# Optimization experiments

Measured on AMD Instinct MI355X. Metric: run time of the kernel, lower is better.

Reference implementation:

```python
import jax, jax.numpy as jnp
import numpy as np

D_MODEL = 512
NUM_HEADS = 8
DEPTH = D_MODEL // NUM_HEADS
BATCH = 2
SEQ = 2048
NEG_INF_SCALE = -1e9


def setup_inputs() -> dict:
    key = jax.random.key(0)
    ks = jax.random.split(key, 9)
    s = 0.02
    return {
        "v": jax.random.normal(ks[0], (BATCH, SEQ, D_MODEL), jnp.float32),
        "q": jax.random.normal(ks[1], (BATCH, SEQ, D_MODEL), jnp.float32),
        "k": jax.random.normal(ks[2], (BATCH, SEQ, D_MODEL), jnp.float32),
        "mask": jax.random.randint(ks[3], (BATCH, 1, SEQ, SEQ), 0, 2, jnp.int32),
        "wq_w": jax.random.normal(ks[4], (D_MODEL, D_MODEL), jnp.float32) * s,
        "wq_b": jnp.zeros((D_MODEL,), jnp.float32),
        "wk_w": jax.random.normal(ks[5], (D_MODEL, D_MODEL), jnp.float32) * s,
        "wk_b": jnp.zeros((D_MODEL,), jnp.float32),
        "wv_w": jax.random.normal(ks[6], (D_MODEL, D_MODEL), jnp.float32) * s,
        "wv_b": jnp.zeros((D_MODEL,), jnp.float32),
        "wo_w": jax.random.normal(ks[7], (D_MODEL, D_MODEL), jnp.float32) * s,
        "wo_b": jnp.zeros((D_MODEL,), jnp.float32),
    }


def _split_heads(x, b):
    # [b, s, d_model] -> [b, h, s, depth]
    return x.reshape(b, -1, NUM_HEADS, DEPTH).transpose(0, 2, 1, 3)


def reference(v, q, k, mask, wq_w, wq_b, wk_w, wk_b, wv_w, wv_b, wo_w, wo_b):
    b = q.shape[0]
    vv = _split_heads(v @ wv_w + wv_b, b)  # [b,h,s,d]
    kk = _split_heads(k @ wk_w + wk_b, b)
    qq = _split_heads(q @ wq_w + wq_b, b)
    # NOTE: the original code swaps q/k at the helper call site, so logits = K @ Q^T.
    logits = jnp.einsum("bhkd,bhqd->bhkq", kk, qq) / jnp.sqrt(jnp.float32(DEPTH))
    logits = logits + mask.astype(jnp.float32) * NEG_INF_SCALE
    attn = jax.nn.softmax(logits, axis=-1)  # softmax over the query axis (faithful quirk)
    # output = A^T @ V  -> [b,h,q,d]
    out = jnp.einsum("bhkq,bhkd->bhqd", attn, vv)
    concat = out.transpose(0, 2, 1, 3).reshape(b, -1, D_MODEL)
    return concat @ wo_w + wo_b, attn
```

## Files before the change

### kernel.cpp

```cpp
#include <hip/hip_runtime.h>

#define S 2048
#define DM 512
#define NH 8
#define HD 64
#define NB 2
#define BH (NB * NH)
#define MROWS (NB * S)
#define QW (S / 32)

typedef __bf16 bf16x8 __attribute__((ext_vector_type(8)));
typedef float f32x4 __attribute__((ext_vector_type(4)));

union FragU {
  uint4 u;
  bf16x8 v;
  unsigned short s[8];
};

__device__ __forceinline__ unsigned short f2bf(float x) {
  unsigned u = __float_as_uint(x);
  u += 0x7FFFu + ((u >> 16) & 1u);
  return (unsigned short)(u >> 16);
}

__global__ __launch_bounds__(256) void k_prep(
    const float* __restrict__ w0, const float* __restrict__ w1,
    const float* __restrict__ w2, const float* __restrict__ w3,
    unsigned short* __restrict__ wt,
    const float* __restrict__ q, const float* __restrict__ k, const float* __restrict__ v,
    unsigned short* __restrict__ oq, unsigned short* __restrict__ ok, unsigned short* __restrict__ ov,
    const int* __restrict__ mask, unsigned* __restrict__ mp,
    float* __restrict__ Zs) {
  __shared__ float tile[64][65];
  int bid = blockIdx.x;
  int tid = threadIdx.x;
  if (bid < 256) {
    int i = bid >> 6, rem = bid & 63;
    const float* w = (i == 0) ? w0 : (i == 1) ? w1 : (i == 2) ? w2 : w3;
    int k0 = (rem & 7) * 64, n0 = (rem >> 3) * 64;
    int tx = tid & 63, ty = tid >> 6;
    for (int r = ty; r < 64; r += 4)
      tile[r][tx] = w[(size_t)(k0 + r) * DM + n0 + tx];
    __syncthreads();
    unsigned short* o = wt + (size_t)i * DM * DM;
    for (int r = ty; r < 64; r += 4)
      o[(size_t)(n0 + r) * DM + k0 + tx] = f2bf(tile[tx][r]);
  } else if (bid < 3328) {
    int b2 = bid - 256;
    int which = b2 >> 10;
    const float* src = (which == 0) ? q : (which == 1) ? k : v;
    unsigned short* dst = (which == 0) ? oq : (which == 1) ? ok : ov;
    size_t t = (size_t)(b2 & 1023) * 256 + tid;
    const float4* s4 = (const float4*)src + t * 2;
    float4 x = s4[0], y = s4[1];
    FragU f;
    f.s[0] = f2bf(x.x); f.s[1] = f2bf(x.y); f.s[2] = f2bf(x.z); f.s[3] = f2bf(x.w);
    f.s[4] = f2bf(y.x); f.s[5] = f2bf(y.y); f.s[6] = f2bf(y.z); f.s[7] = f2bf(y.w);
    *(uint4*)(dst + t * 8) = f.u;
  } else if (bid < 4352) {
    size_t t = (size_t)(bid - 3328) * 256 + tid;
    const int4* mb = (const int4*)(mask + t * 32);
    unsigned bits = 0;
#pragma unroll
    for (int c = 0; c < 8; c++) {
      int4 m = mb[c];
      bits |= (m.x != 0 ? 1u : 0u) << (c * 4);
      bits |= (m.y != 0 ? 1u : 0u) << (c * 4 + 1);
      bits |= (m.z != 0 ? 1u : 0u) << (c * 4 + 2);
      bits |= (m.w != 0 ? 1u : 0u) << (c * 4 + 3);
    }
    mp[t] = bits;
  } else {
    int t = (bid - 4352) * 256 + tid;
    ((float4*)Zs)[t] = make_float4(0.f, 0.f, 0.f, 0.f);
  }
}

__global__ __launch_bounds__(256) void k_proj(
    const unsigned short* __restrict__ inq, const unsigned short* __restrict__ ink,
    const unsigned short* __restrict__ inv, const unsigned short* __restrict__ wt,
    const float* __restrict__ bq, const float* __restrict__ bk, const float* __restrict__ bv,
    unsigned short* __restrict__ oq, unsigned short* __restrict__ ok,
    unsigned short* __restrict__ vvT) {
  __shared__ __align__(16) unsigned short vt[64][72];
  int which = blockIdx.z;
  const unsigned short* in = (which == 0) ? inq : (which == 1) ? ink : inv;
  const float* bias = (which == 0) ? bq : (which == 1) ? bk : bv;
  const unsigned short* w = wt + (size_t)which * DM * DM;

  int lane = threadIdx.x & 63, wv = threadIdx.x >> 6;
  int m0 = blockIdx.x * 64 + wv * 16;
  int n0 = blockIdx.y * 64;
  int kf = (lane >> 4) * 8;
  int arow = m0 + (lane & 15);

  f32x4 acc[4] = {{0.f, 0.f, 0.f, 0.f}, {0.f, 0.f, 0.f, 0.f},
                  {0.f, 0.f, 0.f, 0.f}, {0.f, 0.f, 0.f, 0.f}};

  for (int kk0 = 0; kk0 < DM; kk0 += 32) {
    FragU af;
    af.u = *(const uint4*)(in + (size_t)arow * DM + kk0 + kf);
#pragma unroll
    for (int nt = 0; nt < 4; nt++) {
      FragU bfr;
      bfr.u = *(const uint4*)(w + (size_t)(n0 + nt * 16 + (lane & 15)) * DM + kk0 + kf);
      acc[nt] = __builtin_amdgcn_mfma_f32_16x16x32_bf16(af.v, bfr.v, acc[nt], 0, 0, 0);
    }
  }

  if (which < 2) {
    unsigned short* out = (which == 0) ? oq : ok;
#pragma unroll
    for (int nt = 0; nt < 4; nt++) {
#pragma unroll
      for (int r = 0; r < 4; r++) {
        int row = m0 + (lane >> 4) * 4 + r;
        int col = n0 + nt * 16 + (lane & 15);
        float val = acc[nt][r] + bias[col];
        int b = row >> 11, sIdx = row & (S - 1);
        int h = col >> 6, d = col & 63;
        out[(((size_t)(b * NH + h) * S) + sIdx) * HD + d] = f2bf(val);
      }
    }
  } else {
#pragma unroll
    for (int nt = 0; nt < 4; nt++) {
#pragma unroll
      for (int r = 0; r < 4; r++) {
        int sl = wv * 16 + (lane >> 4) * 4 + r;
        int dl = nt * 16 + (lane & 15);
        vt[dl][sl] = f2bf(acc[nt][r] + bias[n0 + dl]);
      }
    }
    __syncthreads();
    int b = (blockIdx.x * 64) >> 11;
    int s0l = (blockIdx.x * 64) & (S - 1);
    int h = n0 >> 6;
    unsigned short* op = vvT + (size_t)(b * NH + h) * HD * S;
    int d = threadIdx.x >> 2;
    int sc = (threadIdx.x & 3) * 16;
#pragma unroll
    for (int j = 0; j < 2; j++)
      *(uint4*)&op[(size_t)d * S + s0l + sc + j * 8] = *(uint4*)&vt[d][sc + j * 8];
  }
}

__global__ __launch_bounds__(256, 4) void k_softmax_z(
    const unsigned short* __restrict__ qq, const unsigned short* __restrict__ kk,
    const unsigned* __restrict__ mp, float* __restrict__ Zsum) {
  int lane = threadIdx.x & 63, w = threadIdx.x >> 6;
  int bh = blockIdx.y;
  int b = bh >> 3;
  int k0 = blockIdx.x * 64 + w * 16;
  int kf = (lane >> 4) * 8;
  int qbase = blockIdx.z * (S / 2);
  int krow_b = k0 + (lane >> 4) * 4;

  const unsigned short* kbase = kk + ((size_t)bh * S + k0 + (lane & 15)) * HD + kf;
  FragU a0, a1;
  a0.u = *(const uint4*)kbase;
  a1.u = *(const uint4*)(kbase + 32);

  const unsigned short* qbaseP = qq + (size_t)bh * S * HD;
  const unsigned* mpb = mp + (size_t)b * S * QW;

  float sum[4] = {0.f, 0.f, 0.f, 0.f};

  for (int q0 = qbase; q0 < qbase + S / 2; q0 += 64) {
    uint2 mw[4];
#pragma unroll
    for (int r = 0; r < 4; r++)
      mw[r] = *(const uint2*)&mpb[(size_t)(krow_b + r) * QW + (q0 >> 5)];
#pragma unroll
    for (int nt = 0; nt < 4; nt++) {
      int qcol = q0 + nt * 16 + (lane & 15);
      const unsigned short* qp = qbaseP + (size_t)qcol * HD + kf;
      FragU b0, b1;
      b0.u = *(const uint4*)qp;
      b1.u = *(const uint4*)(qp + 32);
      f32x4 c = {0.f, 0.f, 0.f, 0.f};
      c = __builtin_amdgcn_mfma_f32_16x16x32_bf16(a0.v, b0.v, c, 0, 0, 0);
      c = __builtin_amdgcn_mfma_f32_16x16x32_bf16(a1.v, b1.v, c, 0, 0, 0);
      unsigned bpos = (unsigned)(nt * 16 + (lane & 15)) & 31u;
#pragma unroll
      for (int r = 0; r < 4; r++) {
        unsigned word = (nt < 2) ? mw[r].x : mw[r].y;
        float e = __expf(c[r] * 0.125f);
        sum[r] += ((word >> bpos) & 1u) ? 0.f : e;
      }
    }
  }
#pragma unroll
  for (int r = 0; r < 4; r++) {
    float s = sum[r];
    s += __shfl_xor(s, 1);
    s += __shfl_xor(s, 2);
    s += __shfl_xor(s, 4);
    s += __shfl_xor(s, 8);
    if ((lane & 15) == 0)
      atomicAdd(&Zsum[(size_t)bh * S + krow_b + r], s);
  }
}

__global__ __launch_bounds__(256, 4) void k_attn(
    const unsigned short* __restrict__ qq, const unsigned short* __restrict__ kk,
    const unsigned short* __restrict__ vvT, const unsigned* __restrict__ mp,
    const float* __restrict__ Zsum, float* __restrict__ attn_out,
    float* __restrict__ pO) {
  __shared__ __align__(16) unsigned short pT[2][64][72];
  int lane = threadIdx.x & 63, w = threadIdx.x >> 6;
  int bh = blockIdx.y;
  int b = bh >> 3, h = bh & 7;
  int q0 = blockIdx.x * 64;
  int kbase = blockIdx.z * (S / 2);
  int kf = (lane >> 4) * 8;

  FragU bq[4][2];
#pragma unroll
  for (int nt = 0; nt < 4; nt++) {
    const unsigned short* qp = qq + ((size_t)bh * S + q0 + nt * 16 + (lane & 15)) * HD + kf;
    bq[nt][0].u = *(const uint4*)qp;
    bq[nt][1].u = *(const uint4*)(qp + 32);
  }

  f32x4 o[4] = {{0.f, 0.f, 0.f, 0.f}, {0.f, 0.f, 0.f, 0.f},
                {0.f, 0.f, 0.f, 0.f}, {0.f, 0.f, 0.f, 0.f}};

  const unsigned short* kkb = kk + (size_t)bh * S * HD;
  const unsigned short* vb = vvT + (size_t)bh * HD * S;
  const unsigned* mpb = mp + (size_t)b * S * QW;
  float* ao = attn_out + (size_t)bh * S * S;
  const float* zb = Zsum + (size_t)bh * S;
  int q0w = q0 >> 5;

  int buf = 0;
  for (int k0 = kbase; k0 < kbase + S / 2; k0 += 64) {
    int kw = k0 + w * 16;
    int krow_b = kw + (lane >> 4) * 4;
    const unsigned short* kp = kkb + (size_t)(kw + (lane & 15)) * HD + kf;
    FragU a0, a1;
    a0.u = *(const uint4*)kp;
    a1.u = *(const uint4*)(kp + 32);
    float iz[4];
    uint2 mw[4];
#pragma unroll
    for (int r = 0; r < 4; r++) {
      iz[r] = 1.0f / zb[krow_b + r];
      mw[r] = *(const uint2*)&mpb[(size_t)(krow_b + r) * QW + q0w];
    }

#pragma unroll
    for (int nt = 0; nt < 4; nt++) {
      f32x4 c = {0.f, 0.f, 0.f, 0.f};
      c = __builtin_amdgcn_mfma_f32_16x16x32_bf16(a0.v, bq[nt][0].v, c, 0, 0, 0);
      c = __builtin_amdgcn_mfma_f32_16x16x32_bf16(a1.v, bq[nt][1].v, c, 0, 0, 0);
      int ql = nt * 16 + (lane & 15);
      int qcol = q0 + ql;
      unsigned bpos = (unsigned)ql & 31u;
#pragma unroll
      for (int r = 0; r < 4; r++) {
        int kl = w * 16 + (lane >> 4) * 4 + r;
        int krow = k0 + kl;
        unsigned word = (nt < 2) ? mw[r].x : mw[r].y;
        float a = ((word >> bpos) & 1u) ? 0.f : __expf(c[r] * 0.125f) * iz[r];
        ao[(size_t)krow * S + qcol] = a;
        pT[buf][ql][kl] = f2bf(a);
      }
    }
    __syncthreads();
#pragma unroll
    for (int ks = 0; ks < 2; ks++) {
      FragU af;
      af.u = *(const uint4*)(&pT[buf][w * 16 + (lane & 15)][kf + ks * 32]);
#pragma unroll
      for (int nt = 0; nt < 4; nt++) {
        FragU bfr;
        bfr.u = *(const uint4*)(vb + (size_t)(nt * 16 + (lane & 15)) * S + k0 + kf + ks * 32);
        o[nt] = __builtin_amdgcn_mfma_f32_16x16x32_bf16(af.v, bfr.v, o[nt], 0, 0, 0);
      }
    }
    buf ^= 1;
  }

  float* pOz = pO + (size_t)blockIdx.z * MROWS * DM;
#pragma unroll
  for (int nt = 0; nt < 4; nt++) {
#pragma unroll
    for (int r = 0; r < 4; r++) {
      int qg = q0 + w * 16 + (lane >> 4) * 4 + r;
      int col = h * 64 + nt * 16 + (lane & 15);
      pOz[((size_t)b * S + qg) * DM + col] = o[nt][r];
    }
  }
}

__global__ __launch_bounds__(256) void k_reduceO(const float* __restrict__ p0,
                                                  const float* __restrict__ p1,
                                                  unsigned short* __restrict__ conc) {
  size_t t = (size_t)blockIdx.x * 256 + threadIdx.x;
  float4 a = ((const float4*)p0)[t];
  float4 b = ((const float4*)p1)[t];
  union { unsigned short s[4]; uint2 u; } o;
  o.s[0] = f2bf(a.x + b.x);
  o.s[1] = f2bf(a.y + b.y);
  o.s[2] = f2bf(a.z + b.z);
  o.s[3] = f2bf(a.w + b.w);
  *(uint2*)(conc + t * 4) = o.u;
}

__global__ __launch_bounds__(256) void k_outproj(
    const unsigned short* __restrict__ concat, const unsigned short* __restrict__ wt,
    const float* __restrict__ bias, float* __restrict__ out) {
  const unsigned short* w = wt + (size_t)3 * DM * DM;
  int lane = threadIdx.x & 63, wv = threadIdx.x >> 6;
  int m0 = blockIdx.x * 64 + wv * 16;
  int n0 = blockIdx.y * 64;
  int kf = (lane >> 4) * 8;

  f32x4 acc[4] = {{0.f, 0.f, 0.f, 0.f}, {0.f, 0.f, 0.f, 0.f},
                  {0.f, 0.f, 0.f, 0.f}, {0.f, 0.f, 0.f, 0.f}};

  for (int kk0 = 0; kk0 < DM; kk0 += 32) {
    FragU af;
    af.u = *(const uint4*)(concat + (size_t)(m0 + (lane & 15)) * DM + kk0 + kf);
#pragma unroll
    for (int nt = 0; nt < 4; nt++) {
      FragU bfr;
      bfr.u = *(const uint4*)(w + (size_t)(n0 + nt * 16 + (lane & 15)) * DM + kk0 + kf);
      acc[nt] = __builtin_amdgcn_mfma_f32_16x16x32_bf16(af.v, bfr.v, acc[nt], 0, 0, 0);
    }
  }
#pragma unroll
  for (int nt = 0; nt < 4; nt++) {
#pragma unroll
    for (int r = 0; r < 4; r++) {
      int row = m0 + (lane >> 4) * 4 + r;
      int col = n0 + nt * 16 + (lane & 15);
      out[(size_t)row * DM + col] = acc[nt][r] + bias[col];
    }
  }
}

extern "C" void kernel_launch(void* const* d_in, const int* in_sizes, int n_in,
                              void* d_out, int out_size, void* d_ws, size_t ws_size,
                              hipStream_t stream) {
  (void)in_sizes; (void)n_in; (void)out_size; (void)ws_size;
  const float* v    = (const float*)d_in[0];
  const float* q    = (const float*)d_in[1];
  const float* k    = (const float*)d_in[2];
  const int*   mask = (const int*)d_in[3];
  const float* wq_w = (const float*)d_in[4];
  const float* wq_b = (const float*)d_in[5];
  const float* wk_w = (const float*)d_in[6];
  const float* wk_b = (const float*)d_in[7];
  const float* wv_w = (const float*)d_in[8];
  const float* wv_b = (const float*)d_in[9];
  const float* wo_w = (const float*)d_in[10];
  const float* wo_b = (const float*)d_in[11];

  char* ws = (char*)d_ws;
  size_t off = 0;
  auto alloc = [&](size_t bytes) {
    char* p = ws + off;
    off += (bytes + 255) & ~(size_t)255;
    return p;
  };
  unsigned short* wt   = (unsigned short*)alloc((size_t)4 * DM * DM * 2);
  unsigned short* qbf  = (unsigned short*)alloc((size_t)MROWS * DM * 2);
  unsigned short* kbf  = (unsigned short*)alloc((size_t)MROWS * DM * 2);
  unsigned short* vbf  = (unsigned short*)alloc((size_t)MROWS * DM * 2);
  unsigned short* qq   = (unsigned short*)alloc((size_t)BH * S * HD * 2);
  unsigned short* kk2  = (unsigned short*)alloc((size_t)BH * S * HD * 2);
  unsigned short* vvT  = (unsigned short*)alloc((size_t)BH * S * HD * 2);
  unsigned*       mp   = (unsigned*)alloc((size_t)NB * S * QW * 4);
  float*          Zs   = (float*)alloc((size_t)BH * S * 4);
  float*          pO   = (float*)alloc((size_t)2 * MROWS * DM * 4);
  unsigned short* conc = (unsigned short*)alloc((size_t)MROWS * DM * 2);

  float* out_final = (float*)d_out;
  float* out_attn  = (float*)d_out + (size_t)MROWS * DM;

  k_prep<<<dim3(4384), 256, 0, stream>>>(wq_w, wk_w, wv_w, wo_w, wt,
                                          q, k, v, qbf, kbf, vbf,
                                          mask, mp, Zs);
  k_proj<<<dim3(64, 8, 3), 256, 0, stream>>>(qbf, kbf, vbf, wt, wq_b, wk_b, wv_b,
                                              qq, kk2, vvT);
  k_softmax_z<<<dim3(32, 16, 2), 256, 0, stream>>>(qq, kk2, mp, Zs);
  k_attn<<<dim3(32, 16, 2), 256, 0, stream>>>(qq, kk2, vvT, mp, Zs, out_attn, pO);
  k_reduceO<<<dim3(2048), 256, 0, stream>>>(pO, pO + (size_t)MROWS * DM, conc);
  k_outproj<<<dim3(64, 8), 256, 0, stream>>>(conc, wt, wo_b, out_final);
}
```

Baseline: 553.4 us.

## Merge split-K attention halves into one block and drop reduce kernel

```diff
diff --git a/kernel.cpp b/kernel.cpp
--- a/kernel.cpp
+++ b/kernel.cpp
@@ -11,6 +11,8 @@
 
 typedef __bf16 bf16x8 __attribute__((ext_vector_type(8)));
 typedef float f32x4 __attribute__((ext_vector_type(4)));
+typedef float nf4 __attribute__((ext_vector_type(4)));
+typedef int ni4 __attribute__((ext_vector_type(4)));
 
 union FragU {
   uint4 u;
@@ -52,19 +54,20 @@
     const float* src = (which == 0) ? q : (which == 1) ? k : v;
     unsigned short* dst = (which == 0) ? oq : (which == 1) ? ok : ov;
     size_t t = (size_t)(b2 & 1023) * 256 + tid;
-    const float4* s4 = (const float4*)src + t * 2;
-    float4 x = s4[0], y = s4[1];
+    const nf4* s4 = (const nf4*)src + t * 2;
+    nf4 x = __builtin_nontemporal_load(s4);
+    nf4 y = __builtin_nontemporal_load(s4 + 1);
     FragU f;
     f.s[0] = f2bf(x.x); f.s[1] = f2bf(x.y); f.s[2] = f2bf(x.z); f.s[3] = f2bf(x.w);
     f.s[4] = f2bf(y.x); f.s[5] = f2bf(y.y); f.s[6] = f2bf(y.z); f.s[7] = f2bf(y.w);
     *(uint4*)(dst + t * 8) = f.u;
   } else if (bid < 4352) {
     size_t t = (size_t)(bid - 3328) * 256 + tid;
-    const int4* mb = (const int4*)(mask + t * 32);
+    const ni4* mb = (const ni4*)(mask + t * 32);
     unsigned bits = 0;
 #pragma unroll
     for (int c = 0; c < 8; c++) {
-      int4 m = mb[c];
+      ni4 m = __builtin_nontemporal_load(mb + c);
       bits |= (m.x != 0 ? 1u : 0u) << (c * 4);
       bits |= (m.y != 0 ? 1u : 0u) << (c * 4 + 1);
       bits |= (m.z != 0 ? 1u : 0u) << (c * 4 + 2);
@@ -203,17 +206,17 @@
   }
 }
 
-__global__ __launch_bounds__(256, 4) void k_attn(
+__global__ __launch_bounds__(512, 4) void k_attn(
     const unsigned short* __restrict__ qq, const unsigned short* __restrict__ kk,
     const unsigned short* __restrict__ vvT, const unsigned* __restrict__ mp,
     const float* __restrict__ Zsum, float* __restrict__ attn_out,
-    float* __restrict__ pO) {
-  __shared__ __align__(16) unsigned short pT[2][64][72];
+    unsigned short* __restrict__ conc) {
+  __shared__ __align__(16) unsigned short pT[2][2][64][72];
   int lane = threadIdx.x & 63, w = threadIdx.x >> 6;
+  int g = w >> 2, w4 = w & 3;
   int bh = blockIdx.y;
   int b = bh >> 3, h = bh & 7;
   int q0 = blockIdx.x * 64;
-  int kbase = blockIdx.z * (S / 2);
   int kf = (lane >> 4) * 8;
 
   FragU bq[4][2];
@@ -233,10 +236,11 @@
   float* ao = attn_out + (size_t)bh * S * S;
   const float* zb = Zsum + (size_t)bh * S;
   int q0w = q0 >> 5;
+  int kbase = g * (S / 2);
 
   int buf = 0;
   for (int k0 = kbase; k0 < kbase + S / 2; k0 += 64) {
-    int kw = k0 + w * 16;
+    int kw = k0 + w4 * 16;
     int krow_b = kw + (lane >> 4) * 4;
     const unsigned short* kp = kkb + (size_t)(kw + (lane & 15)) * HD + kf;
     FragU a0, a1;
@@ -260,19 +264,19 @@
       unsigned bpos = (unsigned)ql & 31u;
 #pragma unroll
       for (int r = 0; r < 4; r++) {
-        int kl = w * 16 + (lane >> 4) * 4 + r;
+        int kl = w4 * 16 + (lane >> 4) * 4 + r;
         int krow = k0 + kl;
         unsigned word = (nt < 2) ? mw[r].x : mw[r].y;
         float a = ((word >> bpos) & 1u) ? 0.f : __expf(c[r] * 0.125f) * iz[r];
-        ao[(size_t)krow * S + qcol] = a;
-        pT[buf][ql][kl] = f2bf(a);
+        __builtin_nontemporal_store(a, &ao[(size_t)krow * S + qcol]);
+        pT[g][buf][ql][kl] = f2bf(a);
       }
     }
     __syncthreads();
 #pragma unroll
     for (int ks = 0; ks < 2; ks++) {
       FragU af;
-      af.u = *(const uint4*)(&pT[buf][w * 16 + (lane & 15)][kf + ks * 32]);
+      af.u = *(const uint4*)(&pT[g][buf][w4 * 16 + (lane & 15)][kf + ks * 32]);
 #pragma unroll
       for (int nt = 0; nt < 4; nt++) {
         FragU bfr;
@@ -283,30 +287,29 @@
     buf ^= 1;
   }
 
-  float* pOz = pO + (size_t)blockIdx.z * MROWS * DM;
-#pragma unroll
-  for (int nt = 0; nt < 4; nt++) {
-#pragma unroll
-    for (int r = 0; r < 4; r++) {
-      int qg = q0 + w * 16 + (lane >> 4) * 4 + r;
-      int col = h * 64 + nt * 16 + (lane & 15);
-      pOz[((size_t)b * S + qg) * DM + col] = o[nt][r];
-    }
-  }
-}
-
-__global__ __launch_bounds__(256) void k_reduceO(const float* __restrict__ p0,
-                                                  const float* __restrict__ p1,
-                                                  unsigned short* __restrict__ conc) {
-  size_t t = (size_t)blockIdx.x * 256 + threadIdx.x;
-  float4 a = ((const float4*)p0)[t];
-  float4 b = ((const float4*)p1)[t];
-  union { unsigned short s[4]; uint2 u; } o;
-  o.s[0] = f2bf(a.x + b.x);
-  o.s[1] = f2bf(a.y + b.y);
-  o.s[2] = f2bf(a.z + b.z);
-  o.s[3] = f2bf(a.w + b.w);
-  *(uint2*)(conc + t * 4) = o.u;
+  __syncthreads();
+  float* oacc = (float*)&pT[0][0][0][0];
+  int qr = w4 * 16 + (lane >> 4) * 4;
+  if (g == 1) {
+#pragma unroll
+    for (int nt = 0; nt < 4; nt++)
+#pragma unroll
+      for (int r = 0; r < 4; r++)
+        oacc[(qr + r) * 65 + nt * 16 + (lane & 15)] = o[nt][r];
+  }
+  __syncthreads();
+  if (g == 0) {
+#pragma unroll
+    for (int nt = 0; nt < 4; nt++) {
+#pragma unroll
+      for (int r = 0; r < 4; r++) {
+        int qg = q0 + qr + r;
+        int col = h * 64 + nt * 16 + (lane & 15);
+        float s = o[nt][r] + oacc[(qr + r) * 65 + nt * 16 + (lane & 15)];
+        conc[((size_t)(b * S + qg)) * DM + col] = f2bf(s);
+      }
+    }
+  }
 }
 
 __global__ __launch_bounds__(256) void k_outproj(
@@ -375,7 +378,6 @@
   unsigned short* vvT  = (unsigned short*)alloc((size_t)BH * S * HD * 2);
   unsigned*       mp   = (unsigned*)alloc((size_t)NB * S * QW * 4);
   float*          Zs   = (float*)alloc((size_t)BH * S * 4);
-  float*          pO   = (float*)alloc((size_t)2 * MROWS * DM * 4);
   unsigned short* conc = (unsigned short*)alloc((size_t)MROWS * DM * 2);
 
   float* out_final = (float*)d_out;
@@ -387,7 +389,6 @@
   k_proj<<<dim3(64, 8, 3), 256, 0, stream>>>(qbf, kbf, vbf, wt, wq_b, wk_b, wv_b,
                                               qq, kk2, vvT);
   k_softmax_z<<<dim3(32, 16, 2), 256, 0, stream>>>(qq, kk2, mp, Zs);
-  k_attn<<<dim3(32, 16, 2), 256, 0, stream>>>(qq, kk2, vvT, mp, Zs, out_attn, pO);
-  k_reduceO<<<dim3(2048), 256, 0, stream>>>(pO, pO + (size_t)MROWS * DM, conc);
+  k_attn<<<dim3(32, 16), 512, 0, stream>>>(qq, kk2, vvT, mp, Zs, out_attn, conc);
   k_outproj<<<dim3(64, 8), 256, 0, stream>>>(conc, wt, wo_b, out_final);
 }
```

Measured after the change: 536.4 us. 1.03x faster.
